# Kernel optimization log

Hardware: AMD Instinct MI355X
Metric: run time of the kernel (lower is better)

The kernel has to match this reference:

```python
import jax, jax.numpy as jnp
import numpy as np

DIM = 2048
N_HEADS = 32
N_KV_HEADS = 4
HEAD_DIM = DIM // N_HEADS  # 64


def _rope_tables(T, head_dim, dtype):
    inv_freq = 1.0 / (10000.0 ** (jnp.arange(0, head_dim, 2, dtype=jnp.float32) / head_dim))
    t = jnp.arange(T, dtype=jnp.float32)
    freqs = jnp.einsum('i,j->ij', t, inv_freq)           # [T, head_dim/2]
    emb = jnp.concatenate([freqs, freqs], axis=-1)        # [T, head_dim]
    return jnp.cos(emb).astype(dtype), jnp.sin(emb).astype(dtype)


def _rotate_half(x):
    d = x.shape[-1] // 2
    return jnp.concatenate([-x[..., d:], x[..., :d]], axis=-1)


def setup_inputs() -> dict:
    key = jax.random.key(0)
    kx, kq, kk, kv, ko = jax.random.split(key, 5)
    s = 1.0 / np.sqrt(DIM)
    return {
        'x': jax.random.normal(kx, (2, 2048, DIM), dtype=jnp.float32),
        'wq': jax.random.normal(kq, (DIM, DIM), dtype=jnp.float32) * s,
        'wk': jax.random.normal(kk, (DIM, DIM // 8), dtype=jnp.float32) * s,
        'wv': jax.random.normal(kv, (DIM, DIM // 8), dtype=jnp.float32) * s,
        'wo': jax.random.normal(ko, (DIM, DIM), dtype=jnp.float32) * s,
    }


def reference(x, wq, wk, wv, wo):
    B, T, C = x.shape
    q = (x @ wq).reshape(B, T, N_HEADS, HEAD_DIM).transpose(0, 2, 1, 3)      # [B,H,T,D]
    k = (x @ wk).reshape(B, T, N_KV_HEADS, HEAD_DIM).transpose(0, 2, 1, 3)   # [B,Hkv,T,D]
    v = (x @ wv).reshape(B, T, N_KV_HEADS, HEAD_DIM).transpose(0, 2, 1, 3)

    cos, sin = _rope_tables(T, HEAD_DIM, x.dtype)  # [T,D]
    q = q * cos + _rotate_half(q) * sin
    k = k * cos + _rotate_half(k) * sin

    rep = N_HEADS // N_KV_HEADS
    k = jnp.repeat(k, rep, axis=1)  # [B,H,T,D]
    v = jnp.repeat(v, rep, axis=1)

    scale = 1.0 / np.sqrt(HEAD_DIM)
    scores = jnp.einsum('bhqd,bhkd->bhqk', q, k) * scale
    causal = jnp.tril(jnp.ones((T, T), dtype=bool))
    scores = jnp.where(causal, scores, jnp.finfo(scores.dtype).min)
    attn = jax.nn.softmax(scores, axis=-1)
    out = jnp.einsum('bhqk,bhkd->bhqd', attn, v)
    out = out.transpose(0, 2, 1, 3).reshape(B, T, C)
    return out @ wo
```

## Files before the change

### kernel.cpp

```cpp
#include <hip/hip_runtime.h>
#include <hip/hip_bf16.h>
#include <stdint.h>

#define DIM 2048
#define TSEQ 2048
#define BATCH 2
#define NH 32
#define NKV 4
#define HD 64
#define MROWS (BATCH*TSEQ)
#define NQKV 2560

typedef __attribute__((ext_vector_type(4))) float f32x4;
typedef __attribute__((ext_vector_type(8))) __bf16 bf16x8;
typedef unsigned short ushort_t;

#define GLDS16(g, l) __builtin_amdgcn_global_load_lds( \
    (const __attribute__((address_space(1))) void*)(g), \
    (__attribute__((address_space(3))) void*)(l), 16, 0, 0)

__device__ __forceinline__ float bflo2f(unsigned int w) {
  union { unsigned int i; float f; } c; c.i = w << 16; return c.f;
}
__device__ __forceinline__ unsigned short f2bf(float f) {
  union { float f; unsigned int i; } c; c.f = f;
  unsigned int x = c.i;
  x += 0x7fffu + ((x >> 16) & 1u);
  return (unsigned short)(x >> 16);
}
__device__ __forceinline__ unsigned short f2bf_fast(float f) {
  union { float f; unsigned int i; } c; c.f = f;
  return (unsigned short)((c.i + 0x8000u) >> 16);
}

__global__ void cast_bf16_k(const float* __restrict__ in, ushort_t* __restrict__ out, int n4) {
  const int i = blockIdx.x * 256 + threadIdx.x;
  if (i >= n4) return;
  const float4 v = ((const float4*)in)[i];
  uint2 p;
  p.x = (unsigned int)f2bf(v.x) | ((unsigned int)f2bf(v.y) << 16);
  p.y = (unsigned int)f2bf(v.z) | ((unsigned int)f2bf(v.w) << 16);
  ((uint2*)out)[i] = p;
}

__global__ void transpose_cast(const float* __restrict__ w, ushort_t* __restrict__ wt, int K, int N) {
  __shared__ float tile[32][33];
  const int bk = blockIdx.x * 32;
  const int bn = blockIdx.y * 32;
  const int tx = threadIdx.x & 31;
  const int ty = threadIdx.x >> 5;
#pragma unroll
  for (int p = 0; p < 4; p++) {
    const int r = ty + p * 8;
    tile[r][tx] = w[(long)(bk + r) * N + bn + tx];
  }
  __syncthreads();
#pragma unroll
  for (int p = 0; p < 4; p++) {
    const int r = ty + p * 8;
    wt[(long)(bn + r) * K + bk + tx] = f2bf(tile[tx][r]);
  }
}

template<int EPI>
__global__ __launch_bounds__(256, 2) void gemm_bt(
    const ushort_t* __restrict__ A, const ushort_t* __restrict__ BT,
    int M, int N, int K,
    float* __restrict__ Cf, ushort_t* __restrict__ Cq,
    ushort_t* __restrict__ Ck, ushort_t* __restrict__ Cv)
{
  __shared__ __align__(16) ushort_t As[128][64];
  __shared__ __align__(16) ushort_t Bs[128][64];
  const int tid  = threadIdx.x;
  const int lane = tid & 63;
  const int wid  = tid >> 6;
  const int wm   = wid >> 1, wn = wid & 1;
  const int l8   = lane >> 3;
  const int c8   = (lane & 7) * 8;
  const long abase = (long)blockIdx.x * 128 * K;
  const long bbase = (long)blockIdx.y * 128 * K;
  const int rsel = lane & 15;
  const int koff = (lane >> 4) * 8;
  f32x4 acc[4][4] = {};

  for (int k0 = 0; k0 < K; k0 += 64) {
    __syncthreads();
#pragma unroll
    for (int i = 0; i < 4; i++) {
      const int r0 = wid * 32 + i * 8;
      GLDS16(&A [abase + (long)(r0 + l8) * K + k0 + c8], &As[r0][0]);
      GLDS16(&BT[bbase + (long)(r0 + l8) * K + k0 + c8], &Bs[r0][0]);
    }
    __syncthreads();
#pragma unroll
    for (int kk = 0; kk < 64; kk += 32) {
      bf16x8 af[4], bfr[4];
#pragma unroll
      for (int m = 0; m < 4; m++) af[m]  = *(const bf16x8*)(&As[wm*64 + m*16 + rsel][kk + koff]);
#pragma unroll
      for (int n = 0; n < 4; n++) bfr[n] = *(const bf16x8*)(&Bs[wn*64 + n*16 + rsel][kk + koff]);
#pragma unroll
      for (int m = 0; m < 4; m++)
#pragma unroll
        for (int n = 0; n < 4; n++)
          acc[m][n] = __builtin_amdgcn_mfma_f32_16x16x32_bf16(af[m], bfr[n], acc[m][n], 0, 0, 0);
    }
  }

  const int rbase = blockIdx.x * 128 + wm * 64 + (lane >> 4) * 4;
  const int cbase = blockIdx.y * 128 + wn * 64 + (lane & 15);
#pragma unroll
  for (int m = 0; m < 4; m++) {
#pragma unroll
    for (int n = 0; n < 4; n++) {
      const int gn = cbase + n * 16;
#pragma unroll
      for (int j = 0; j < 4; j++) {
        const int gm = rbase + m * 16 + j;
        const float v = acc[m][n][j];
        if (EPI == 1) {
          Cf[(long)gm * N + gn] = v;
        } else {
          if (gn < DIM) {
            Cq[(long)gm * DIM + gn] = f2bf(v);
          } else {
            const int x = gn - DIM;
            const int hkv = (x >> 6) & 3;
            const int d = x & 63;
            const int b = gm >> 11;
            const int t = gm & (TSEQ - 1);
            if (x < 256) Ck[((long)(b * NKV + hkv) * TSEQ + t) * HD + d] = f2bf(v);
            else         Cv[((long)(b * NKV + hkv) * HD + d) * TSEQ + t] = f2bf(v);
          }
        }
      }
    }
  }
}

#define LOG1E4_D32 0.2878231366242557f
#define QSCALE 0.1803368801111243f

__global__ void rope_q_k(ushort_t* __restrict__ q) {
  const int idx = blockIdx.x * 256 + threadIdx.x;
  const int m  = idx >> 10;
  const int rr = idx & 1023;
  const int h  = rr >> 5;
  const int d  = rr & 31;
  const int t  = m & (TSEQ - 1);
  const float ang = (float)t * __expf(-(float)d * LOG1E4_D32);
  float s_, c_;
  __sincosf(ang, &s_, &c_);
  const long base = (long)m * DIM + h * 64 + d;
  const float q0 = bflo2f(q[base]);
  const float q1 = bflo2f(q[base + 32]);
  q[base]      = f2bf((q0 * c_ - q1 * s_) * QSCALE);
  q[base + 32] = f2bf((q1 * c_ + q0 * s_) * QSCALE);
}

__global__ void rope_k_k(ushort_t* __restrict__ k) {
  const int idx = blockIdx.x * 256 + threadIdx.x;
  const int row = idx >> 5;
  const int d   = idx & 31;
  const int t   = row & (TSEQ - 1);
  const float ang = (float)t * __expf(-(float)d * LOG1E4_D32);
  float s_, c_;
  __sincosf(ang, &s_, &c_);
  const long base = (long)row * HD + d;
  const float k0 = bflo2f(k[base]);
  const float k1 = bflo2f(k[base + 32]);
  k[base]      = f2bf(k0 * c_ - k1 * s_);
  k[base + 32] = f2bf(k1 * c_ + k0 * s_);
}

__global__ __launch_bounds__(512, 6) void attn_mfma(
    const ushort_t* __restrict__ q, const ushort_t* __restrict__ k,
    const ushort_t* __restrict__ vt, ushort_t* __restrict__ o)
{
  __shared__ __align__(16) ushort_t Ks[2][64][64];
  __shared__ __align__(16) ushort_t Vs[2][64][64];
  __shared__ __align__(16) ushort_t Ps[8][16][64];

  const int tid  = threadIdx.x;
  const int lane = tid & 63;
  const int wid  = tid >> 6;
  const int l15  = lane & 15;
  const int lg   = lane >> 4;
  const int sw   = l15 & 7;

  const int bh  = blockIdx.x & 63;
  const int qt  = (TSEQ / 128 - 1) - (blockIdx.x >> 6);
  const int h   = bh & (NH - 1);
  const int b   = bh >> 5;
  const int hkv = h >> 3;
  const int qbase = qt * 128;
  const int qw0   = qbase + wid * 16;

  bf16x8 qf[2];
  {
    const ushort_t* qp = q + ((long)(b * TSEQ) + qw0 + l15) * DIM + h * 64 + lg * 8;
    qf[0] = *(const bf16x8*)(qp);
    qf[1] = *(const bf16x8*)(qp + 32);
  }

  const ushort_t* kb_ = k  + (long)(b * NKV + hkv) * TSEQ * HD;
  const ushort_t* vb_ = vt + (long)(b * NKV + hkv) * HD * TSEQ;

  float m_g = -1e30f;
  float l_c = 0.f;
  f32x4 o_[4] = {};

  const int srow = tid >> 3;
  const int sgc  = (tid & 7) * 8;
  const int slc  = (((tid & 7) ^ (srow & 7))) * 8;

  const int nkv = 2 * (qt + 1);

  *(uint4*)(&Ks[0][srow][slc]) = *(const uint4*)(&kb_[(long)srow * HD + sgc]);
  *(uint4*)(&Vs[0][srow][slc]) = *(const uint4*)(&vb_[(long)srow * TSEQ + sgc]);
  int cur = 0;

  for (int kbv = 0; kbv < nkv; kbv++) {
    const int kb0 = kbv * 64;
    const bool pf = (kbv + 1 < nkv);
    uint4 kr = {}, vr = {};
    if (pf) {
      kr = *(const uint4*)(&kb_[(long)(kb0 + 64 + srow) * HD + sgc]);
      vr = *(const uint4*)(&vb_[(long)srow * TSEQ + kb0 + 64 + sgc]);
    }
    asm volatile("s_waitcnt lgkmcnt(0)\n\ts_barrier" ::: "memory");

    if (kb0 <= qw0 + 15) {
      f32x4 st[4] = {};
#pragma unroll
      for (int kt = 0; kt < 4; kt++) {
#pragma unroll
        for (int c = 0; c < 2; c++) {
          const bf16x8 kf = *(const bf16x8*)(&Ks[cur][kt * 16 + l15][((4*c + lg) ^ sw) * 8]);
          st[kt] = __builtin_amdgcn_mfma_f32_16x16x32_bf16(kf, qf[c], st[kt], 0, 0, 0);
        }
      }

      if (kb0 + 63 > qw0) {
        const int qg = qw0 + l15;
#pragma unroll
        for (int kt = 0; kt < 4; kt++) {
          const int kg0 = kb0 + kt * 16 + lg * 4;
#pragma unroll
          for (int j = 0; j < 4; j++) {
            if (kg0 + j > qg) st[kt][j] = -1e30f;
          }
        }
      }

      float pm;
      {
        float mk0 = fmaxf(fmaxf(st[0][0], st[0][1]), fmaxf(st[0][2], st[0][3]));
        float mk1 = fmaxf(fmaxf(st[1][0], st[1][1]), fmaxf(st[1][2], st[1][3]));
        float mk2 = fmaxf(fmaxf(st[2][0], st[2][1]), fmaxf(st[2][2], st[2][3]));
        float mk3 = fmaxf(fmaxf(st[3][0], st[3][1]), fmaxf(st[3][2], st[3][3]));
        pm = fmaxf(fmaxf(mk0, mk1), fmaxf(mk2, mk3));
      }
      pm = fmaxf(pm, __shfl_xor(pm, 16, 64));
      pm = fmaxf(pm, __shfl_xor(pm, 32, 64));

      if (__any(pm > m_g + 8.f)) {
        const float mnew = fmaxf(m_g, pm);
        const float alc  = exp2f(m_g - mnew);
        m_g = mnew;
        l_c *= alc;
        float alr[4];
#pragma unroll
        for (int j = 0; j < 4; j++)
          alr[j] = __shfl(alc, (lane & 48) | (lg * 4 + j), 64);
#pragma unroll
        for (int nt = 0; nt < 4; nt++)
#pragma unroll
          for (int j = 0; j < 4; j++) o_[nt][j] *= alr[j];
      }

      float rs = 0.f;
#pragma unroll
      for (int kt = 0; kt < 4; kt++) {
        const float p0 = exp2f(st[kt][0] - m_g);
        const float p1 = exp2f(st[kt][1] - m_g);
        const float p2 = exp2f(st[kt][2] - m_g);
        const float p3 = exp2f(st[kt][3] - m_g);
        rs += (p0 + p1) + (p2 + p3);
        unsigned int d0, d1;
        asm("v_cvt_pk_bf16_f32 %0, %1, %2" : "=v"(d0) : "v"(p0), "v"(p1));
        asm("v_cvt_pk_bf16_f32 %0, %1, %2" : "=v"(d1) : "v"(p2), "v"(p3));
        const int g0 = ((2 * kt + (lg >> 1)) ^ sw) * 8 + (lg & 1) * 4;
        *(unsigned int*)(&Ps[wid][l15][g0])     = d0;
        *(unsigned int*)(&Ps[wid][l15][g0 + 2]) = d1;
      }
      rs += __shfl_xor(rs, 16, 64);
      rs += __shfl_xor(rs, 32, 64);
      l_c += rs;

#pragma unroll
      for (int c = 0; c < 2; c++) {
        const bf16x8 pa = *(const bf16x8*)(&Ps[wid][l15][((4*c + lg) ^ sw) * 8]);
#pragma unroll
        for (int nt = 0; nt < 4; nt++) {
          const bf16x8 vf = *(const bf16x8*)(&Vs[cur][nt * 16 + l15][((4*c + lg) ^ sw) * 8]);
          o_[nt] = __builtin_amdgcn_mfma_f32_16x16x32_bf16(pa, vf, o_[nt], 0, 0, 0);
        }
      }
    }

    if (pf) {
      *(uint4*)(&Ks[cur ^ 1][srow][slc]) = kr;
      *(uint4*)(&Vs[cur ^ 1][srow][slc]) = vr;
    }
    cur ^= 1;
  }

  const long orow = (long)(b * TSEQ) + qw0;
#pragma unroll
  for (int j = 0; j < 4; j++) {
    const float inv = 1.f / __shfl(l_c, (lane & 48) | (lg * 4 + j), 64);
#pragma unroll
    for (int nt = 0; nt < 4; nt++)
      o[(orow + lg * 4 + j) * DIM + h * 64 + nt * 16 + l15] = f2bf_fast(o_[nt][j] * inv);
  }
}

extern "C" void kernel_launch(void* const* d_in, const int* in_sizes, int n_in,
                              void* d_out, int out_size, void* d_ws, size_t ws_size,
                              hipStream_t stream) {
  const float* x  = (const float*)d_in[0];
  const float* wq = (const float*)d_in[1];
  const float* wk = (const float*)d_in[2];
  const float* wv = (const float*)d_in[3];
  const float* wo = (const float*)d_in[4];
  float* out = (float*)d_out;

  ushort_t* ws = (ushort_t*)d_ws;
  const long NXB = (long)MROWS * DIM;
  ushort_t* xb   = ws;
  ushort_t* wtq  = xb  + NXB;
  ushort_t* woT  = wtq + (long)NQKV * DIM;
  ushort_t* qws  = woT + (long)DIM * DIM;
  ushort_t* kws  = qws + NXB;
  ushort_t* vtws = kws + (long)BATCH * NKV * TSEQ * HD;
  ushort_t* aws  = vtws + (long)BATCH * NKV * TSEQ * HD;

  cast_bf16_k<<<(int)(NXB / 1024), 256, 0, stream>>>(x, xb, (int)(NXB / 4));
  transpose_cast<<<dim3(64, 64), 256, 0, stream>>>(wq, wtq, DIM, DIM);
  transpose_cast<<<dim3(64, 8),  256, 0, stream>>>(wk, wtq + (long)DIM  * DIM, DIM, 256);
  transpose_cast<<<dim3(64, 8),  256, 0, stream>>>(wv, wtq + (long)2304 * DIM, DIM, 256);
  transpose_cast<<<dim3(64, 64), 256, 0, stream>>>(wo, woT, DIM, DIM);

  gemm_bt<0><<<dim3(32, 20), 256, 0, stream>>>(xb, wtq, MROWS, NQKV, DIM,
                                               nullptr, qws, kws, vtws);
  rope_q_k<<<(MROWS * NH * 32) / 256, 256, 0, stream>>>(qws);
  rope_k_k<<<(BATCH * NKV * TSEQ * 32) / 256, 256, 0, stream>>>(kws);

  attn_mfma<<<BATCH * NH * (TSEQ / 128), 512, 0, stream>>>(qws, kws, vtws, aws);

  gemm_bt<1><<<dim3(32, 16), 256, 0, stream>>>(aws, woT, MROWS, DIM, DIM,
                                               out, nullptr, nullptr, nullptr);
}
```

Before: 226.7 us.

## Merge prep launches, keep P in registers via lane shuffles, raise attention occupancy

The four weight transpose-cast launches are merged into one grid, and the two RoPE kernels into one launch, to cut launch overhead and tail gaps. In attention, the softmax probabilities are no longer staged through per-wave LDS. They are rearranged into the MFMA A-operand layout with cross-lane shuffles, which removes LDS writes and reads and frees LDS. The launch bound rises from 6 to 8 waves-per-EU hint, which may force register pressure or spills.

```diff
diff --git a/kernel.cpp b/kernel.cpp
--- a/kernel.cpp
+++ b/kernel.cpp
@@ -43,22 +43,30 @@
   ((uint2*)out)[i] = p;
 }
 
-__global__ void transpose_cast(const float* __restrict__ w, ushort_t* __restrict__ wt, int K, int N) {
+__global__ void transpose_cast_all(const float* __restrict__ wq, const float* __restrict__ wk,
+                                   const float* __restrict__ wv, const float* __restrict__ wo,
+                                   ushort_t* __restrict__ wtq, ushort_t* __restrict__ woT) {
   __shared__ float tile[32][33];
+  const int by = blockIdx.y;
+  const float* src; ushort_t* dst; int N, bnb;
+  if (by < 64)      { src = wq; dst = wtq;                    N = DIM; bnb = by; }
+  else if (by < 72) { src = wk; dst = wtq + (long)DIM  * DIM; N = 256; bnb = by - 64; }
+  else if (by < 80) { src = wv; dst = wtq + (long)2304 * DIM; N = 256; bnb = by - 72; }
+  else              { src = wo; dst = woT;                    N = DIM; bnb = by - 80; }
   const int bk = blockIdx.x * 32;
-  const int bn = blockIdx.y * 32;
+  const int bn = bnb * 32;
   const int tx = threadIdx.x & 31;
   const int ty = threadIdx.x >> 5;
 #pragma unroll
   for (int p = 0; p < 4; p++) {
     const int r = ty + p * 8;
-    tile[r][tx] = w[(long)(bk + r) * N + bn + tx];
+    tile[r][tx] = src[(long)(bk + r) * N + bn + tx];
   }
   __syncthreads();
 #pragma unroll
   for (int p = 0; p < 4; p++) {
     const int r = ty + p * 8;
-    wt[(long)(bn + r) * K + bk + tx] = f2bf(tile[tx][r]);
+    dst[(long)(bn + r) * DIM + bk + tx] = f2bf(tile[tx][r]);
   }
 }
 
@@ -140,52 +148,54 @@
 
 #define LOG1E4_D32 0.2878231366242557f
 #define QSCALE 0.1803368801111243f
-
-__global__ void rope_q_k(ushort_t* __restrict__ q) {
-  const int idx = blockIdx.x * 256 + threadIdx.x;
-  const int m  = idx >> 10;
-  const int rr = idx & 1023;
-  const int h  = rr >> 5;
-  const int d  = rr & 31;
-  const int t  = m & (TSEQ - 1);
-  const float ang = (float)t * __expf(-(float)d * LOG1E4_D32);
-  float s_, c_;
-  __sincosf(ang, &s_, &c_);
-  const long base = (long)m * DIM + h * 64 + d;
-  const float q0 = bflo2f(q[base]);
-  const float q1 = bflo2f(q[base + 32]);
-  q[base]      = f2bf((q0 * c_ - q1 * s_) * QSCALE);
-  q[base + 32] = f2bf((q1 * c_ + q0 * s_) * QSCALE);
-}
-
-__global__ void rope_k_k(ushort_t* __restrict__ k) {
-  const int idx = blockIdx.x * 256 + threadIdx.x;
-  const int row = idx >> 5;
-  const int d   = idx & 31;
-  const int t   = row & (TSEQ - 1);
-  const float ang = (float)t * __expf(-(float)d * LOG1E4_D32);
-  float s_, c_;
-  __sincosf(ang, &s_, &c_);
-  const long base = (long)row * HD + d;
-  const float k0 = bflo2f(k[base]);
-  const float k1 = bflo2f(k[base + 32]);
-  k[base]      = f2bf(k0 * c_ - k1 * s_);
-  k[base + 32] = f2bf(k1 * c_ + k0 * s_);
-}
-
-__global__ __launch_bounds__(512, 6) void attn_mfma(
+#define NQBLK ((MROWS * NH * 32) / 256)
+
+__global__ void rope_all(ushort_t* __restrict__ q, ushort_t* __restrict__ k) {
+  if (blockIdx.x < NQBLK) {
+    const int idx = blockIdx.x * 256 + threadIdx.x;
+    const int m  = idx >> 10;
+    const int rr = idx & 1023;
+    const int h  = rr >> 5;
+    const int d  = rr & 31;
+    const int t  = m & (TSEQ - 1);
+    const float ang = (float)t * __expf(-(float)d * LOG1E4_D32);
+    float s_, c_;
+    __sincosf(ang, &s_, &c_);
+    const long base = (long)m * DIM + h * 64 + d;
+    const float q0 = bflo2f(q[base]);
+    const float q1 = bflo2f(q[base + 32]);
+    q[base]      = f2bf((q0 * c_ - q1 * s_) * QSCALE);
+    q[base + 32] = f2bf((q1 * c_ + q0 * s_) * QSCALE);
+  } else {
+    const int idx = (blockIdx.x - NQBLK) * 256 + threadIdx.x;
+    const int row = idx >> 5;
+    const int d   = idx & 31;
+    const int t   = row & (TSEQ - 1);
+    const float ang = (float)t * __expf(-(float)d * LOG1E4_D32);
+    float s_, c_;
+    __sincosf(ang, &s_, &c_);
+    const long base = (long)row * HD + d;
+    const float k0 = bflo2f(k[base]);
+    const float k1 = bflo2f(k[base + 32]);
+    k[base]      = f2bf(k0 * c_ - k1 * s_);
+    k[base + 32] = f2bf(k1 * c_ + k0 * s_);
+  }
+}
+
+__global__ __launch_bounds__(512, 8) void attn_mfma(
     const ushort_t* __restrict__ q, const ushort_t* __restrict__ k,
     const ushort_t* __restrict__ vt, ushort_t* __restrict__ o)
 {
   __shared__ __align__(16) ushort_t Ks[2][64][64];
   __shared__ __align__(16) ushort_t Vs[2][64][64];
-  __shared__ __align__(16) ushort_t Ps[8][16][64];
 
   const int tid  = threadIdx.x;
   const int lane = tid & 63;
   const int wid  = tid >> 6;
   const int l15  = lane & 15;
   const int lg   = lane >> 4;
+  const int od   = lg & 1;
+  const int hi   = lg >> 1;
   const int sw   = l15 & 7;
 
   const int bh  = blockIdx.x & 63;
@@ -214,6 +224,9 @@
   const int sgc  = (tid & 7) * 8;
   const int slc  = (((tid & 7) ^ (srow & 7))) * 8;
 
+  const int gv0 = ((0 + 2 * od + hi) ^ sw) * 8;
+  const int gv1 = ((4 + 2 * od + hi) ^ sw) * 8;
+
   const int nkv = 2 * (qt + 1);
 
   *(uint4*)(&Ks[0][srow][slc]) = *(const uint4*)(&kb_[(long)srow * HD + sgc]);
@@ -280,32 +293,44 @@
       }
 
       float rs = 0.f;
-#pragma unroll
-      for (int kt = 0; kt < 4; kt++) {
-        const float p0 = exp2f(st[kt][0] - m_g);
-        const float p1 = exp2f(st[kt][1] - m_g);
-        const float p2 = exp2f(st[kt][2] - m_g);
-        const float p3 = exp2f(st[kt][3] - m_g);
-        rs += (p0 + p1) + (p2 + p3);
-        unsigned int d0, d1;
-        asm("v_cvt_pk_bf16_f32 %0, %1, %2" : "=v"(d0) : "v"(p0), "v"(p1));
-        asm("v_cvt_pk_bf16_f32 %0, %1, %2" : "=v"(d1) : "v"(p2), "v"(p3));
-        const int g0 = ((2 * kt + (lg >> 1)) ^ sw) * 8 + (lg & 1) * 4;
-        *(unsigned int*)(&Ps[wid][l15][g0])     = d0;
-        *(unsigned int*)(&Ps[wid][l15][g0 + 2]) = d1;
-      }
+      unsigned int u00, u01, u10, u11, u20, u21, u30, u31;
+#define PACK_KT(KT, UA, UB) { \
+        const float p0 = exp2f(st[KT][0] - m_g); \
+        const float p1 = exp2f(st[KT][1] - m_g); \
+        const float p2 = exp2f(st[KT][2] - m_g); \
+        const float p3 = exp2f(st[KT][3] - m_g); \
+        rs += (p0 + p1) + (p2 + p3); \
+        asm("v_cvt_pk_bf16_f32 %0, %1, %2" : "=v"(UA) : "v"(p0), "v"(p1)); \
+        asm("v_cvt_pk_bf16_f32 %0, %1, %2" : "=v"(UB) : "v"(p2), "v"(p3)); \
+      }
+      PACK_KT(0, u00, u01)
+      PACK_KT(1, u10, u11)
+      PACK_KT(2, u20, u21)
+      PACK_KT(3, u30, u31)
+#undef PACK_KT
       rs += __shfl_xor(rs, 16, 64);
       rs += __shfl_xor(rs, 32, 64);
       l_c += rs;
 
-#pragma unroll
-      for (int c = 0; c < 2; c++) {
-        const bf16x8 pa = *(const bf16x8*)(&Ps[wid][l15][((4*c + lg) ^ sw) * 8]);
-#pragma unroll
-        for (int nt = 0; nt < 4; nt++) {
-          const bf16x8 vf = *(const bf16x8*)(&Vs[cur][nt * 16 + l15][((4*c + lg) ^ sw) * 8]);
-          o_[nt] = __builtin_amdgcn_mfma_f32_16x16x32_bf16(pa, vf, o_[nt], 0, 0, 0);
-        }
+      const unsigned int r00 = __shfl_xor((int)(od ? u00 : u10), 16, 64);
+      const unsigned int r01 = __shfl_xor((int)(od ? u01 : u11), 16, 64);
+      const unsigned int r10 = __shfl_xor((int)(od ? u20 : u30), 16, 64);
+      const unsigned int r11 = __shfl_xor((int)(od ? u21 : u31), 16, 64);
+      union { unsigned int u[4]; bf16x8 v; } T0, T1;
+      T0.u[0] = od ? r00 : u00;  T0.u[1] = od ? r01 : u01;
+      T0.u[2] = od ? u10 : r00;  T0.u[3] = od ? u11 : r01;
+      T1.u[0] = od ? r10 : u20;  T1.u[1] = od ? r11 : u21;
+      T1.u[2] = od ? u30 : r10;  T1.u[3] = od ? u31 : r11;
+
+#pragma unroll
+      for (int nt = 0; nt < 4; nt++) {
+        const bf16x8 vf0 = *(const bf16x8*)(&Vs[cur][nt * 16 + l15][gv0]);
+        o_[nt] = __builtin_amdgcn_mfma_f32_16x16x32_bf16(T0.v, vf0, o_[nt], 0, 0, 0);
+      }
+#pragma unroll
+      for (int nt = 0; nt < 4; nt++) {
+        const bf16x8 vf1 = *(const bf16x8*)(&Vs[cur][nt * 16 + l15][gv1]);
+        o_[nt] = __builtin_amdgcn_mfma_f32_16x16x32_bf16(T1.v, vf1, o_[nt], 0, 0, 0);
       }
     }
 
@@ -347,15 +372,11 @@
   ushort_t* aws  = vtws + (long)BATCH * NKV * TSEQ * HD;
 
   cast_bf16_k<<<(int)(NXB / 1024), 256, 0, stream>>>(x, xb, (int)(NXB / 4));
-  transpose_cast<<<dim3(64, 64), 256, 0, stream>>>(wq, wtq, DIM, DIM);
-  transpose_cast<<<dim3(64, 8),  256, 0, stream>>>(wk, wtq + (long)DIM  * DIM, DIM, 256);
-  transpose_cast<<<dim3(64, 8),  256, 0, stream>>>(wv, wtq + (long)2304 * DIM, DIM, 256);
-  transpose_cast<<<dim3(64, 64), 256, 0, stream>>>(wo, woT, DIM, DIM);
+  transpose_cast_all<<<dim3(64, 144), 256, 0, stream>>>(wq, wk, wv, wo, wtq, woT);
 
   gemm_bt<0><<<dim3(32, 20), 256, 0, stream>>>(xb, wtq, MROWS, NQKV, DIM,
                                                nullptr, qws, kws, vtws);
-  rope_q_k<<<(MROWS * NH * 32) / 256, 256, 0, stream>>>(qws);
-  rope_k_k<<<(BATCH * NKV * TSEQ * 32) / 256, 256, 0, stream>>>(kws);
+  rope_all<<<NQBLK + (BATCH * NKV * TSEQ * 32) / 256, 256, 0, stream>>>(qws, kws);
 
   attn_mfma<<<BATCH * NH * (TSEQ / 128), 512, 0, stream>>>(qws, kws, vtws, aws);
 
```

New measurement: 247.8 us. +9.3%, slower.
